# Optimization experiments

Measured on AMD Instinct MI355X. Metric: run time of the kernel, lower is better.

The kernel has to match this reference:

```python
import jax, jax.numpy as jnp
import numpy as np

D_MODEL = 1024
D_HIDDEN = 4096
BATCH = 4
SEQ = 2048
EPS = 1e-5
SLOPE = 0.01  # LeakyReLU default negative_slope


def layer_norm(x, g, b):
    m = jnp.mean(x, axis=-1, keepdims=True)
    v = jnp.mean(jnp.square(x - m), axis=-1, keepdims=True)
    return (x - m) * jax.lax.rsqrt(v + EPS) * g + b


def leaky_relu(x):
    return jnp.where(x >= 0, x, SLOPE * x)


def setup_inputs() -> dict:
    key = jax.random.key(0)
    ks = jax.random.split(key, 8)
    scale = D_MODEL ** 0.5
    x = jax.random.normal(ks[0], (BATCH, SEQ, D_MODEL), dtype=jnp.float32)
    qk = jax.random.normal(ks[1], (D_MODEL, D_MODEL), dtype=jnp.float32) / scale
    ov = jax.random.normal(ks[2], (D_MODEL, D_MODEL), dtype=jnp.float32) / scale
    ln1_g = jnp.ones((D_MODEL,), jnp.float32)
    ln1_b = jnp.zeros((D_MODEL,), jnp.float32)
    ln2_g = jnp.ones((D_MODEL,), jnp.float32)
    ln2_b = jnp.zeros((D_MODEL,), jnp.float32)
    # nn.Linear default init: uniform(-1/sqrt(fan_in), 1/sqrt(fan_in))
    def lin(k, fan_in, fan_out):
        k1, k2 = jax.random.split(k)
        bd = 1.0 / np.sqrt(fan_in)
        W = jax.random.uniform(k1, (fan_out, fan_in), jnp.float32, -bd, bd)
        b = jax.random.uniform(k2, (fan_out,), jnp.float32, -bd, bd)
        return W, b
    W_up, b_up = lin(ks[3], D_MODEL, D_HIDDEN)
    W_h, b_h = lin(ks[4], D_HIDDEN, D_HIDDEN)
    W_down, b_down = lin(ks[5], D_HIDDEN, D_MODEL)
    return {"x": x, "qk": qk, "ov": ov, "ln1_g": ln1_g, "ln1_b": ln1_b,
            "ln2_g": ln2_g, "ln2_b": ln2_b, "W_up": W_up, "b_up": b_up,
            "W_h": W_h, "b_h": b_h, "W_down": W_down, "b_down": b_down}


def reference(x, qk, ov, ln1_g, ln1_b, ln2_g, ln2_b,
              W_up, b_up, W_h, b_h, W_down, b_down):
    scale = D_MODEL ** 0.5
    # --- attention on ln1(x) ---
    h = layer_norm(x, ln1_g, ln1_b)                     # [B,S,D]
    scores = jnp.einsum('bsd,de,bte->bst', h, qk, h) / scale  # [B,S,S]
    n = h.shape[1]
    causal = jnp.tril(jnp.ones((n, n), bool))
    scores = jnp.where(causal, scores, -jnp.inf)
    probs = jax.nn.softmax(scores, axis=-1)
    attn = jnp.einsum('bst,btd,de->bse', probs, h, ov)  # [B,S,D]
    x = x + attn
    # --- MLP on ln2(x) ---
    h2 = layer_norm(x, ln2_g, ln2_b)
    a = leaky_relu(h2 @ W_up.T + b_up)
    a = leaky_relu(a @ W_h.T + b_h)
    a = leaky_relu(a @ W_down.T + b_down)
    return x + a
```

## Files before the change

kernel.cpp:

```cpp
#include <hip/hip_runtime.h>
#include <stdint.h>


typedef __attribute__((ext_vector_type(4))) float  f32x4;
typedef __attribute__((ext_vector_type(8))) __bf16 bf16v8;
typedef __attribute__((ext_vector_type(8))) unsigned short u16x8;
typedef unsigned short ushort_t;
typedef unsigned int   u32;

#define SLOPE 0.01f

__device__ __forceinline__ ushort_t f2bf(float f) {
  u32 u = __builtin_bit_cast(u32, f);
  u32 r = (u + 0x7FFFu + ((u >> 16) & 1u)) >> 16;
  return (ushort_t)r;
}
__device__ __forceinline__ float bf2f(ushort_t b) {
  u32 u = ((u32)b) << 16;
  return __builtin_bit_cast(float, u);
}

__device__ __forceinline__ void gload_lds16(const void* g, void* l) {
  __builtin_amdgcn_global_load_lds(
      (const __attribute__((address_space(1))) u32*)g,
      (__attribute__((address_space(3))) u32*)l, 16, 0, 0);
}

template<int EPI, bool CAUSAL>
__global__ __launch_bounds__(512, 1)
void gemm_nt8(const ushort_t* __restrict__ A, const ushort_t* __restrict__ B,
              void* __restrict__ Cv, const float* __restrict__ bias,
              int M, int N, int K, long sAb, long sBb, long sCb)
{
  extern __shared__ char smem[];
  const ushort_t* lds = (const ushort_t*)smem;
  const int tid = threadIdx.x;
  const int l   = tid & 63;
  const int nwg = gridDim.x * gridDim.y;
  const int orig = blockIdx.y * gridDim.x + blockIdx.x;
  const int q8 = nwg >> 3, r8 = nwg & 7;
  const int xcd = orig & 7, io = orig >> 3;
  const int logical = (xcd < r8 ? xcd * (q8 + 1) : r8 * (q8 + 1) + (xcd - r8) * q8) + io;
  const int m0 = (logical / gridDim.x) * 256;
  const int n0 = (logical % gridDim.x) * 256;
  if (CAUSAL && n0 > m0 + 255) return;
  A += (long)blockIdx.z * sAb;
  B += (long)blockIdx.z * sBb;
  const long coff = (long)blockIdx.z * sCb;
  const int wid = tid >> 6;
  const int wm = (wid >> 2) * 128;
  const int wn = (wid & 3) * 64;
  const int nt = K >> 5;

  const int  sg      = (((tid & 3) ^ ((tid >> 3) & 3))) * 8;
  const long rowA0   = (long)(m0 +       (tid >> 2)) * K;
  const long rowA1   = (long)(m0 + 128 + (tid >> 2)) * K;
  const long rowB0   = (long)(n0 +       (tid >> 2)) * K;
  const long rowB1   = (long)(n0 + 128 + (tid >> 2)) * K;
  const int  wbase16 = (tid & ~63) * 16;

#define STAGE(TT) do {                                                        \
    const long _k  = (long)(TT) * 32;                                         \
    char* _ra = (char*)smem + ((TT) & 3) * 32768 + wbase16;                   \
    char* _rb = _ra + 16384;                                                  \
    gload_lds16(A + rowA0 + _k + sg, _ra);                                    \
    gload_lds16(A + rowA1 + _k + sg, _ra + 8192);                             \
    gload_lds16(B + rowB0 + _k + sg, _rb);                                    \
    gload_lds16(B + rowB1 + _k + sg, _rb + 8192);                             \
  } while (0)

  const int fr  = l & 15;
  const int fsl = (((l >> 4) ^ ((l >> 1) & 3))) * 8;

  f32x4 acc[8][4] = {};

  STAGE(0);
  if (nt > 1) STAGE(1);
  if (nt > 2) STAGE(2);
  if (nt > 2)      { asm volatile("s_waitcnt vmcnt(8)" ::: "memory"); }
  else if (nt > 1) { asm volatile("s_waitcnt vmcnt(4)" ::: "memory"); }
  else             { asm volatile("s_waitcnt vmcnt(0)" ::: "memory"); }
  __builtin_amdgcn_s_barrier();
  __builtin_amdgcn_sched_barrier(0);

  for (int t = 0; t < nt; ++t) {
    const int buf = t & 3;
    const ushort_t* rA = lds + buf * 16384 +        (wm + fr) * 32 + fsl;
    const ushort_t* rB = lds + buf * 16384 + 8192 + (wn + fr) * 32 + fsl;
    bf16v8 av[8], bv[4];
#pragma unroll
    for (int mf = 0; mf < 8; mf++) av[mf] = *(const bf16v8*)(rA + mf * 512);
#pragma unroll
    for (int nf = 0; nf < 4; nf++) bv[nf] = *(const bf16v8*)(rB + nf * 512);

    if (t + 3 < nt) STAGE(t + 3);

    __builtin_amdgcn_s_setprio(1);
#pragma unroll
    for (int mf = 0; mf < 8; mf++)
#pragma unroll
      for (int nf = 0; nf < 4; nf++)
        acc[mf][nf] = __builtin_amdgcn_mfma_f32_16x16x32_bf16(
            av[mf], bv[nf], acc[mf][nf], 0, 0, 0);
    __builtin_amdgcn_s_setprio(0);

    if (t <= nt - 4) {
      asm volatile("s_waitcnt vmcnt(8)" ::: "memory");
      __builtin_amdgcn_s_barrier();
      __builtin_amdgcn_sched_barrier(0);
    } else if (t == nt - 3) {
      asm volatile("s_waitcnt vmcnt(4)" ::: "memory");
      __builtin_amdgcn_s_barrier();
      __builtin_amdgcn_sched_barrier(0);
    } else if (t == nt - 2) {
      asm volatile("s_waitcnt vmcnt(0)" ::: "memory");
      __builtin_amdgcn_s_barrier();
      __builtin_amdgcn_sched_barrier(0);
    }
  }
#undef STAGE

  const int lr = (l >> 4) * 4;
#pragma unroll
  for (int mf = 0; mf < 8; mf++) {
    const int row0 = m0 + wm + mf * 16 + lr;
#pragma unroll
    for (int nf = 0; nf < 4; nf++) {
      const int col = n0 + wn + nf * 16 + fr;
      const float bcol = (EPI == 2) ? bias[col] : 0.f;
#pragma unroll
      for (int r = 0; r < 4; r++) {
        float v = acc[mf][nf][r];
        if constexpr (EPI == 2) {
          v += bcol;
          v = v >= 0.f ? v : SLOPE * v;
          ((ushort_t*)Cv)[coff + (long)(row0 + r) * N + col] = f2bf(v);
        } else {
          ((ushort_t*)Cv)[coff + (long)(row0 + r) * N + col] = f2bf(v);
        }
      }
    }
  }
}

template<int EPI, bool KLIM>
__global__ __launch_bounds__(512, 1)
void gemm_nt8b(const ushort_t* __restrict__ A, const ushort_t* __restrict__ B,
               void* __restrict__ Cv, const float* __restrict__ bias,
               const float* __restrict__ resid,
               int M, int N, int K, long sAb, long sBb, long sCb)
{
  extern __shared__ char smem[];
  const ushort_t* lds = (const ushort_t*)smem;
  const int tid = threadIdx.x;
  const int l   = tid & 63;
  const int nwg = gridDim.x * gridDim.y;
  const int orig = blockIdx.y * gridDim.x + blockIdx.x;
  const int q8 = nwg >> 3, r8 = nwg & 7;
  const int xcd = orig & 7, io = orig >> 3;
  const int logical = (xcd < r8 ? xcd * (q8 + 1) : r8 * (q8 + 1) + (xcd - r8) * q8) + io;
  const int m0 = (logical / gridDim.x) * 256;
  const int n0 = (logical % gridDim.x) * 128;
  A += (long)blockIdx.z * sAb;
  B += (long)blockIdx.z * sBb;
  const long coff = (long)blockIdx.z * sCb;
  const int wid = tid >> 6;
  const int wm = (wid >> 1) * 64;
  const int wn = (wid & 1) * 64;
  int Keff = K;
  if (KLIM) Keff = min(K, m0 + 256);
  const int nt = Keff >> 5;

  const int  sg      = (((tid & 3) ^ ((tid >> 3) & 3))) * 8;
  const long rowA0   = (long)(m0 +       (tid >> 2)) * K;
  const long rowA1   = (long)(m0 + 128 + (tid >> 2)) * K;
  const long rowB0   = (long)(n0 +       (tid >> 2)) * K;
  const int  wbase16 = (tid & ~63) * 16;

#define STAGEB(TT) do {                                                       \
    const long _k  = (long)(TT) * 32;                                         \
    char* _ra = (char*)smem + ((TT) & 3) * 24576 + wbase16;                   \
    char* _rb = _ra + 16384;                                                  \
    gload_lds16(A + rowA0 + _k + sg, _ra);                                    \
    gload_lds16(A + rowA1 + _k + sg, _ra + 8192);                             \
    gload_lds16(B + rowB0 + _k + sg, _rb);                                    \
  } while (0)

  const int fr  = l & 15;
  const int fsl = (((l >> 4) ^ ((l >> 1) & 3))) * 8;

  f32x4 acc[4][4] = {};

  STAGEB(0);
  if (nt > 1) STAGEB(1);
  if (nt > 2) STAGEB(2);
  if (nt > 2)      { asm volatile("s_waitcnt vmcnt(6)" ::: "memory"); }
  else if (nt > 1) { asm volatile("s_waitcnt vmcnt(3)" ::: "memory"); }
  else             { asm volatile("s_waitcnt vmcnt(0)" ::: "memory"); }
  __builtin_amdgcn_s_barrier();
  __builtin_amdgcn_sched_barrier(0);

  for (int t = 0; t < nt; ++t) {
    const int buf = t & 3;
    const ushort_t* rA = lds + buf * 12288 +        (wm + fr) * 32 + fsl;
    const ushort_t* rB = lds + buf * 12288 + 8192 + (wn + fr) * 32 + fsl;
    bf16v8 av[4], bv[4];
#pragma unroll
    for (int mf = 0; mf < 4; mf++) av[mf] = *(const bf16v8*)(rA + mf * 512);
#pragma unroll
    for (int nf = 0; nf < 4; nf++) bv[nf] = *(const bf16v8*)(rB + nf * 512);

    if (t + 3 < nt) STAGEB(t + 3);

    __builtin_amdgcn_s_setprio(1);
#pragma unroll
    for (int mf = 0; mf < 4; mf++)
#pragma unroll
      for (int nf = 0; nf < 4; nf++)
        acc[mf][nf] = __builtin_amdgcn_mfma_f32_16x16x32_bf16(
            av[mf], bv[nf], acc[mf][nf], 0, 0, 0);
    __builtin_amdgcn_s_setprio(0);

    if (t <= nt - 4) {
      asm volatile("s_waitcnt vmcnt(6)" ::: "memory");
      __builtin_amdgcn_s_barrier();
      __builtin_amdgcn_sched_barrier(0);
    } else if (t == nt - 3) {
      asm volatile("s_waitcnt vmcnt(3)" ::: "memory");
      __builtin_amdgcn_s_barrier();
      __builtin_amdgcn_sched_barrier(0);
    } else if (t == nt - 2) {
      asm volatile("s_waitcnt vmcnt(0)" ::: "memory");
      __builtin_amdgcn_s_barrier();
      __builtin_amdgcn_sched_barrier(0);
    }
  }
#undef STAGEB

  const int lr = (l >> 4) * 4;
#pragma unroll
  for (int mf = 0; mf < 4; mf++) {
    const int row0 = m0 + wm + mf * 16 + lr;
#pragma unroll
    for (int nf = 0; nf < 4; nf++) {
      const int col = n0 + wn + nf * 16 + fr;
      const float bcol = (EPI == 4) ? bias[col] : 0.f;
#pragma unroll
      for (int r = 0; r < 4; r++) {
        float v = acc[mf][nf][r];
        const long idx = coff + (long)(row0 + r) * N + col;
        if constexpr (EPI == 0) {
          ((ushort_t*)Cv)[idx] = f2bf(v);
        } else if constexpr (EPI == 3) {
          ((float*)Cv)[idx] = v + resid[idx];
        } else {
          v += bcol;
          v = v >= 0.f ? v : SLOPE * v;
          ((float*)Cv)[idx] = v + resid[idx];
        }
      }
    }
  }
}

template<int EPI, bool CAUSAL, bool KLIM>
__global__ __launch_bounds__(256)
void gemm_nt(const ushort_t* __restrict__ A, const ushort_t* __restrict__ B,
             void* __restrict__ Cv, const float* __restrict__ bias,
             const float* __restrict__ resid,
             int M, int N, int K, long sAb, long sBb, long sCb)
{
  __shared__ ushort_t lA[128 * 32];
  __shared__ ushort_t lB[128 * 32];
  const int tid = threadIdx.x;
  const int w = tid >> 6;
  const int l = tid & 63;
  const int nwg = gridDim.x * gridDim.y;
  const int orig = blockIdx.y * gridDim.x + blockIdx.x;
  const int q8 = nwg >> 3, r8 = nwg & 7;
  const int xcd = orig & 7, io = orig >> 3;
  const int logical = (xcd < r8 ? xcd * (q8 + 1) : r8 * (q8 + 1) + (xcd - r8) * q8) + io;
  const int m0 = (logical / gridDim.x) * 128;
  const int n0 = (logical % gridDim.x) * 128;
  if (CAUSAL && n0 > m0 + 127) return;
  const long bz = blockIdx.z;
  A += bz * sAb;
  B += bz * sBb;
  int Keff = K;
  if (KLIM) Keff = min(K, m0 + 128);

  const ushort_t* gA = A + (long)(m0 + w * 32 + (l >> 2)) * K + (l & 3) * 8;
  const ushort_t* gB = B + (long)(n0 + w * 32 + (l >> 2)) * K + (l & 3) * 8;
  ushort_t* lAw0 = &lA[(w * 32) * 32];
  ushort_t* lAw1 = &lA[(w * 32 + 16) * 32];
  ushort_t* lBw0 = &lB[(w * 32) * 32];
  ushort_t* lBw1 = &lB[(w * 32 + 16) * 32];
  const int wm = (w >> 1) * 64, wn = (w & 1) * 64;

  f32x4 acc[4][4] = {};

  for (int k0 = 0; k0 < Keff; k0 += 32) {
    gload_lds16(gA,                 lAw0);
    gload_lds16(gA + (long)16 * K,  lAw1);
    gload_lds16(gB,                 lBw0);
    gload_lds16(gB + (long)16 * K,  lBw1);
    gA += 32; gB += 32;
    __syncthreads();

    bf16v8 af[4], bfr[4];
#pragma unroll
    for (int m = 0; m < 4; m++)
      af[m] = *(const bf16v8*)&lA[(wm + m * 16 + (l & 15)) * 32 + (l >> 4) * 8];
#pragma unroll
    for (int n = 0; n < 4; n++)
      bfr[n] = *(const bf16v8*)&lB[(wn + n * 16 + (l & 15)) * 32 + (l >> 4) * 8];
#pragma unroll
    for (int m = 0; m < 4; m++)
#pragma unroll
      for (int n = 0; n < 4; n++)
        acc[m][n] = __builtin_amdgcn_mfma_f32_16x16x32_bf16(af[m], bfr[n], acc[m][n], 0, 0, 0);
    __syncthreads();
  }

  const int lr = (l >> 4) * 4;
  const int lc = l & 15;
#pragma unroll
  for (int m = 0; m < 4; m++) {
    const int row0 = m0 + wm + m * 16 + lr;
#pragma unroll
    for (int n = 0; n < 4; n++) {
      const int col = n0 + wn + n * 16 + lc;
#pragma unroll
      for (int r = 0; r < 4; r++) {
        float v = acc[m][n][r];
        const long idx = bz * sCb + (long)(row0 + r) * N + col;
        if constexpr (EPI == 0) {
          ((ushort_t*)Cv)[idx] = f2bf(v);
        } else if constexpr (EPI == 2) {
          v += bias[col];
          v = v >= 0.f ? v : SLOPE * v;
          ((ushort_t*)Cv)[idx] = f2bf(v);
        } else if constexpr (EPI == 3) {
          ((float*)Cv)[idx] = v + resid[idx];
        } else {
          v += bias[col];
          v = v >= 0.f ? v : SLOPE * v;
          ((float*)Cv)[idx] = v + resid[idx];
        }
      }
    }
  }
}

__global__ __launch_bounds__(256)
void ln_kernel(const float* __restrict__ x, const float* __restrict__ g,
               const float* __restrict__ bta, ushort_t* __restrict__ o)
{
  const long row = blockIdx.x;
  const int tid = threadIdx.x;
  const float4 v = *((const float4*)(x + row * 1024) + tid);
  float s  = v.x + v.y + v.z + v.w;
  float ss = v.x * v.x + v.y * v.y + v.z * v.z + v.w * v.w;
  for (int o2 = 32; o2 > 0; o2 >>= 1) {
    s  += __shfl_down(s, o2);
    ss += __shfl_down(ss, o2);
  }
  __shared__ float rs[4], rss[4];
  const int w = tid >> 6, l = tid & 63;
  if (l == 0) { rs[w] = s; rss[w] = ss; }
  __syncthreads();
  if (tid == 0) {
    float a = 0, c = 0;
    for (int i = 0; i < 4; i++) { a += rs[i]; c += rss[i]; }
    rs[0] = a; rss[0] = c;
  }
  __syncthreads();
  const float mean = rs[0] * (1.f / 1024.f);
  const float var  = rss[0] * (1.f / 1024.f) - mean * mean;
  const float rstd = rsqrtf(var + 1e-5f);
  const int c0 = tid * 4;
  ushort_t* orow = o + row * 1024;
  const float* vp = (const float*)&v;
#pragma unroll
  for (int i = 0; i < 4; i++)
    orow[c0 + i] = f2bf((vp[i] - mean) * rstd * g[c0 + i] + bta[c0 + i]);
}

__global__ __launch_bounds__(256)
void softmax_kernel(ushort_t* __restrict__ sc)
{
  const long row = blockIdx.x;
  const int s = (int)(row & 2047);
  const int tid = threadIdx.x;
  ushort_t* srow = sc + row * 2048;
  const int t0 = tid * 8;
  u16x8 raw = *(const u16x8*)(srow + t0);
  float v[8];
  const float rsc = 1.0f / 32.0f;
  float mx = -3e38f;
#pragma unroll
  for (int i = 0; i < 8; i++) {
    float f = bf2f(raw[i]) * rsc;
    v[i] = (t0 + i <= s) ? f : -3e38f;
    mx = fmaxf(mx, v[i]);
  }
  for (int o = 32; o > 0; o >>= 1) mx = fmaxf(mx, __shfl_down(mx, o));
  __shared__ float red[8];
  const int w = tid >> 6, l = tid & 63;
  if (l == 0) red[w] = mx;
  __syncthreads();
  if (tid == 0) {
    float m2 = red[0];
    for (int i = 1; i < 4; i++) m2 = fmaxf(m2, red[i]);
    red[0] = m2;
  }
  __syncthreads();
  const float m = red[0];
  float sum = 0.f;
#pragma unroll
  for (int i = 0; i < 8; i++) {
    float e = (t0 + i <= s) ? __expf(v[i] - m) : 0.f;
    v[i] = e; sum += e;
  }
  for (int o = 32; o > 0; o >>= 1) sum += __shfl_down(sum, o);
  if (l == 0) red[4 + w] = sum;
  __syncthreads();
  if (tid == 0) {
    float s2 = 0;
    for (int i = 0; i < 4; i++) s2 += red[4 + i];
    red[0] = 1.0f / s2;
  }
  __syncthreads();
  const float inv = red[0];
#pragma unroll
  for (int i = 0; i < 8; i++) srow[t0 + i] = f2bf(v[i] * inv);
}

__global__ __launch_bounds__(256)
void cast3_bf16(const float* __restrict__ a, const float* __restrict__ b,
                const float* __restrict__ c, ushort_t* __restrict__ oa,
                ushort_t* __restrict__ ob, ushort_t* __restrict__ oc)
{
  long i = ((long)blockIdx.x * 256 + threadIdx.x) * 4;
  const float* src; ushort_t* dst;
  if (i < 4194304L)        { src = a; dst = oa; }
  else if (i < 8388608L)   { src = b + (0 - 4194304L); dst = ob - 4194304L; }
  else                     { src = c + (0 - 8388608L); dst = oc - 8388608L; }
  float4 v = *(const float4*)(src + i);
  dst[i]     = f2bf(v.x);
  dst[i + 1] = f2bf(v.y);
  dst[i + 2] = f2bf(v.z);
  dst[i + 3] = f2bf(v.w);
}

__global__ __launch_bounds__(256)
void transpose_cast2(const float* __restrict__ s0, ushort_t* __restrict__ d0,
                     const float* __restrict__ s1, ushort_t* __restrict__ d1)
{
  __shared__ ushort_t t[32][33];
  const float* in = blockIdx.z ? s1 : s0;
  ushort_t*    o  = blockIdx.z ? d1 : d0;
  const int tx = threadIdx.x & 31, ty = threadIdx.x >> 5;
  const int r0 = blockIdx.y * 32, c0 = blockIdx.x * 32;
#pragma unroll
  for (int i = 0; i < 4; i++)
    t[ty + i * 8][tx] = f2bf(in[(long)(r0 + ty + i * 8) * 1024 + c0 + tx]);
  __syncthreads();
#pragma unroll
  for (int i = 0; i < 4; i++)
    o[(long)(c0 + ty + i * 8) * 1024 + r0 + tx] = t[tx][ty + i * 8];
}

__global__ __launch_bounds__(256)
void transpose_bf16(const ushort_t* __restrict__ in, ushort_t* __restrict__ o,
                    int R, int C)
{
  __shared__ ushort_t t[32][33];
  const long bz = blockIdx.z;
  in += bz * (long)R * C;
  o  += bz * (long)R * C;
  const int tx = threadIdx.x & 31, ty = threadIdx.x >> 5;
  const int r0 = blockIdx.y * 32, c0 = blockIdx.x * 32;
#pragma unroll
  for (int i = 0; i < 4; i++)
    t[ty + i * 8][tx] = in[(long)(r0 + ty + i * 8) * C + c0 + tx];
  __syncthreads();
#pragma unroll
  for (int i = 0; i < 4; i++)
    o[(long)(c0 + ty + i * 8) * R + r0 + tx] = t[tx][ty + i * 8];
}

extern "C" void kernel_launch(void* const* d_in, const int* in_sizes, int n_in,
                              void* d_out, int out_size, void* d_ws, size_t ws_size,
                              hipStream_t stream)
{
  const float* x      = (const float*)d_in[0];
  const float* qk     = (const float*)d_in[1];
  const float* ov     = (const float*)d_in[2];
  const float* ln1_g  = (const float*)d_in[3];
  const float* ln1_b  = (const float*)d_in[4];
  const float* ln2_g  = (const float*)d_in[5];
  const float* ln2_b  = (const float*)d_in[6];
  const float* W_up   = (const float*)d_in[7];
  const float* b_up   = (const float*)d_in[8];
  const float* W_h    = (const float*)d_in[9];
  const float* b_h    = (const float*)d_in[10];
  const float* W_down = (const float*)d_in[11];
  const float* b_down = (const float*)d_in[12];
  float* out = (float*)d_out;
  char* ws = (char*)d_ws;
  const long MB = 1024L * 1024L;

  ushort_t* wqT    = (ushort_t*)(ws +   0 * MB);
  ushort_t* woT    = (ushort_t*)(ws +   2 * MB);
  ushort_t* h      = (ushort_t*)(ws +   4 * MB);
  ushort_t* hT     = (ushort_t*)(ws +  20 * MB);
  ushort_t* q      = (ushort_t*)(ws +  36 * MB);
  ushort_t* scores = (ushort_t*)(ws +  52 * MB);
  ushort_t* h2     = h;
  ushort_t* attnh  = q;
  ushort_t* wu     = hT;
  ushort_t* wd     = (ushort_t*)(ws +  28 * MB);
  ushort_t* wh     = q;
  ushort_t* a1     = (ushort_t*)(ws +  68 * MB);
  ushort_t* a2c    = (ushort_t*)(ws + 100 * MB);
  ushort_t* a2f    = (ushort_t*)(ws + 132 * MB);

  const bool ws197 = ws_size >= (size_t)(197 * MB);
  const bool ws166 = ws_size >= (size_t)(166 * MB);

  transpose_cast2<<<dim3(32, 32, 2), 256, 0, stream>>>(qk, wqT, ov, woT);
  ln_kernel<<<8192, 256, 0, stream>>>(x, ln1_g, ln1_b, h);
  transpose_bf16<<<dim3(32, 64, 4), 256, 0, stream>>>(h, hT, 2048, 1024);

  gemm_nt8b<0, false><<<dim3(8, 32, 1), 512, 98304, stream>>>(
      h, wqT, q, nullptr, nullptr, 8192, 1024, 1024, 0, 0, 0);
  gemm_nt8<0, true><<<dim3(8, 8, 4), 512, 131072, stream>>>(
      q, h, scores, nullptr, 2048, 2048, 1024,
      2048L * 1024, 2048L * 1024, 2048L * 2048);
  softmax_kernel<<<8192, 256, 0, stream>>>(scores);
  gemm_nt8b<0, true><<<dim3(8, 8, 4), 512, 98304, stream>>>(
      scores, hT, attnh, nullptr, nullptr, 2048, 1024, 2048,
      2048L * 2048, 1024L * 2048, 2048L * 1024);
  gemm_nt8b<3, false><<<dim3(8, 32, 1), 512, 98304, stream>>>(
      attnh, woT, out, nullptr, x, 8192, 1024, 1024, 0, 0, 0);

  ln_kernel<<<8192, 256, 0, stream>>>(out, ln2_g, ln2_b, h2);
  cast3_bf16<<<24576, 256, 0, stream>>>(W_up, W_down, W_h, wu, wd, wh);

  if (ws197) {
    gemm_nt8<2, false><<<dim3(16, 32, 1), 512, 131072, stream>>>(
        h2, wu, a1, b_up, 8192, 4096, 1024, 0, 0, 0);
    gemm_nt8<2, false><<<dim3(16, 32, 1), 512, 131072, stream>>>(
        a1, wh, a2f, b_h, 8192, 4096, 4096, 0, 0, 0);
    gemm_nt8b<4, false><<<dim3(8, 32, 1), 512, 98304, stream>>>(
        a2f, wd, out, b_down, out, 8192, 1024, 4096, 0, 0, 0);
  } else if (ws166) {
    for (int c = 0; c < 2; c++) {
      const long r0 = (long)c * 4096;
      gemm_nt8<2, false><<<dim3(16, 16, 1), 512, 131072, stream>>>(
          h2 + r0 * 1024, wu, a1, b_up, 4096, 4096, 1024, 0, 0, 0);
      gemm_nt8<2, false><<<dim3(16, 16, 1), 512, 131072, stream>>>(
          a1, wh, a2c + r0 * 4096, b_h, 4096, 4096, 4096, 0, 0, 0);
    }
    gemm_nt<4, false, false><<<dim3(8, 64, 1), 256, 0, stream>>>(
        a2c, wd, out, b_down, out, 8192, 1024, 4096, 0, 0, 0);
  } else {
    for (int c = 0; c < 2; c++) {
      const long r0 = (long)c * 4096;
      gemm_nt8<2, false><<<dim3(16, 16, 1), 512, 131072, stream>>>(
          h2 + r0 * 1024, wu, a1, b_up, 4096, 4096, 1024, 0, 0, 0);
      gemm_nt8<2, false><<<dim3(16, 16, 1), 512, 131072, stream>>>(
          a1, wh, a2c, b_h, 4096, 4096, 4096, 0, 0, 0);
      gemm_nt<4, false, false><<<dim3(8, 32, 1), 256, 0, stream>>>(
          a2c, wd, out + r0 * 1024, b_down, out + r0 * 1024, 4096, 1024, 4096, 0, 0, 0);
    }
  }
}
```

Baseline: 578.6 us.

## Split GEMM main loop into two half-phases interleaving A/B loads with MFMA

The K-loop of the bf16 GEMM kernel now runs in two phases per iteration. Each phase reads half of the A fragments from LDS, issues half of the next global-to-LDS prefetch (A in the first phase, B in the second), and then runs half of the MFMAs. The aim is to interleave memory issue with matrix work across waves, in the style of ping-pong scheduling, so load issue is spread out and hidden better. It adds extra s_barrier calls per iteration, which can add synchronisation stalls.

Result: slower. 591.7 us (+2.3%).

```diff
diff --git a/kernel.cpp b/kernel.cpp
--- a/kernel.cpp
+++ b/kernel.cpp
@@ -59,12 +59,15 @@
   const long rowB1   = (long)(n0 + 128 + (tid >> 2)) * K;
   const int  wbase16 = (tid & ~63) * 16;
 
-#define STAGE(TT) do {                                                        \
+#define STAGE_AH(TT) do {                                                     \
     const long _k  = (long)(TT) * 32;                                         \
     char* _ra = (char*)smem + ((TT) & 3) * 32768 + wbase16;                   \
-    char* _rb = _ra + 16384;                                                  \
     gload_lds16(A + rowA0 + _k + sg, _ra);                                    \
     gload_lds16(A + rowA1 + _k + sg, _ra + 8192);                             \
+  } while (0)
+#define STAGE_BH(TT) do {                                                     \
+    const long _k  = (long)(TT) * 32;                                         \
+    char* _rb = (char*)smem + ((TT) & 3) * 32768 + 16384 + wbase16;           \
     gload_lds16(B + rowB0 + _k + sg, _rb);                                    \
     gload_lds16(B + rowB1 + _k + sg, _rb + 8192);                             \
   } while (0)
@@ -74,9 +77,9 @@
 
   f32x4 acc[8][4] = {};
 
-  STAGE(0);
-  if (nt > 1) STAGE(1);
-  if (nt > 2) STAGE(2);
+  STAGE_AH(0); STAGE_BH(0);
+  if (nt > 1) { STAGE_AH(1); STAGE_BH(1); }
+  if (nt > 2) { STAGE_AH(2); STAGE_BH(2); }
   if (nt > 2)      { asm volatile("s_waitcnt vmcnt(8)" ::: "memory"); }
   else if (nt > 1) { asm volatile("s_waitcnt vmcnt(4)" ::: "memory"); }
   else             { asm volatile("s_waitcnt vmcnt(0)" ::: "memory"); }
@@ -88,16 +91,34 @@
     const ushort_t* rA = lds + buf * 16384 +        (wm + fr) * 32 + fsl;
     const ushort_t* rB = lds + buf * 16384 + 8192 + (wn + fr) * 32 + fsl;
     bf16v8 av[8], bv[4];
-#pragma unroll
-    for (int mf = 0; mf < 8; mf++) av[mf] = *(const bf16v8*)(rA + mf * 512);
+
+#pragma unroll
+    for (int mf = 0; mf < 4; mf++) av[mf] = *(const bf16v8*)(rA + mf * 512);
 #pragma unroll
     for (int nf = 0; nf < 4; nf++) bv[nf] = *(const bf16v8*)(rB + nf * 512);
-
-    if (t + 3 < nt) STAGE(t + 3);
-
+    if (t + 3 < nt) STAGE_AH(t + 3);
+    __builtin_amdgcn_s_barrier();
+    asm volatile("s_waitcnt lgkmcnt(0)" ::: "memory");
+    __builtin_amdgcn_sched_barrier(0);
     __builtin_amdgcn_s_setprio(1);
 #pragma unroll
-    for (int mf = 0; mf < 8; mf++)
+    for (int mf = 0; mf < 4; mf++)
+#pragma unroll
+      for (int nf = 0; nf < 4; nf++)
+        acc[mf][nf] = __builtin_amdgcn_mfma_f32_16x16x32_bf16(
+            av[mf], bv[nf], acc[mf][nf], 0, 0, 0);
+    __builtin_amdgcn_s_setprio(0);
+    __builtin_amdgcn_s_barrier();
+
+#pragma unroll
+    for (int mf = 4; mf < 8; mf++) av[mf] = *(const bf16v8*)(rA + mf * 512);
+    if (t + 3 < nt) STAGE_BH(t + 3);
+    __builtin_amdgcn_s_barrier();
+    asm volatile("s_waitcnt lgkmcnt(0)" ::: "memory");
+    __builtin_amdgcn_sched_barrier(0);
+    __builtin_amdgcn_s_setprio(1);
+#pragma unroll
+    for (int mf = 4; mf < 8; mf++)
 #pragma unroll
       for (int nf = 0; nf < 4; nf++)
         acc[mf][nf] = __builtin_amdgcn_mfma_f32_16x16x32_bf16(
@@ -118,7 +139,8 @@
       __builtin_amdgcn_sched_barrier(0);
     }
   }
-#undef STAGE
+#undef STAGE_AH
+#undef STAGE_BH
 
   const int lr = (l >> 4) * 4;
 #pragma unroll
```
